# Kernel tuning notes

Measured on AMD Instinct MI355X. Metric: run time of the kernel, lower is better.

## Reference

```python
import jax, jax.numpy as jnp
import numpy as np

D_MODEL = 1024
N_LAYERS = 2
D_STATE = 64
D_CONV = 4
EXPAND = 2
D_INNER = EXPAND * D_MODEL            # 2048
HEADDIM = D_STATE                     # 64 (headdim=d_state per module code)
NHEADS = D_INNER // HEADDIM           # 32
CONV_DIM = D_INNER + 2 * D_STATE      # 2176 (ngroups=1)
D_IN_PROJ = 2 * D_INNER + 2 * D_STATE + NHEADS  # 4256
EPS = 1e-5


def setup_inputs() -> dict:
    key = jax.random.key(0)
    ks = jax.random.split(key, 8)
    B, L = 2, 4096
    return {
        "x": jax.random.normal(ks[0], (B, L, D_MODEL), jnp.float32),
        "ln_w": jnp.ones((N_LAYERS, D_MODEL), jnp.float32),
        "ln_b": jnp.zeros((N_LAYERS, D_MODEL), jnp.float32),
        "in_proj_w": jax.random.normal(ks[1], (N_LAYERS, D_IN_PROJ, D_MODEL), jnp.float32) * (D_MODEL ** -0.5),
        "conv_w": jax.random.normal(ks[2], (N_LAYERS, CONV_DIM, D_CONV), jnp.float32) * (D_CONV ** -0.5),
        "conv_b": jnp.zeros((N_LAYERS, CONV_DIM), jnp.float32),
        "dt_bias": jax.random.normal(ks[3], (N_LAYERS, NHEADS), jnp.float32) * 0.5,
        "A_log": jnp.log(jax.random.uniform(ks[4], (N_LAYERS, NHEADS), jnp.float32, 1.0, 16.0)),
        "D": jnp.ones((N_LAYERS, NHEADS), jnp.float32),
        "rms_w": jnp.ones((N_LAYERS, D_INNER), jnp.float32),
        "out_proj_w": jax.random.normal(ks[5], (N_LAYERS, D_MODEL, D_INNER), jnp.float32) * (D_INNER ** -0.5),
    }


def _layernorm(x, w, b):
    m = x.mean(-1, keepdims=True)
    v = ((x - m) ** 2).mean(-1, keepdims=True)
    return (x - m) * jax.lax.rsqrt(v + EPS) * w + b


def _mamba2(u, in_w, conv_w, conv_b, dt_bias, A_log, Dp, rms_w, out_w):
    b, l, _ = u.shape
    zxbcdt = u @ in_w.T                                   # (b,l,D_IN_PROJ)
    z, xBC, dt = jnp.split(zxbcdt, [D_INNER, D_INNER + CONV_DIM], axis=-1)
    dt = jax.nn.softplus(dt + dt_bias)                    # (b,l,H)
    # causal depthwise conv over sequence
    xBC = jnp.transpose(xBC, (0, 2, 1))                   # (b,C,l)
    xBC = jax.lax.conv_general_dilated(
        xBC, conv_w[:, None, :], (1,), [(D_CONV - 1, 0)],
        dimension_numbers=("NCH", "OIH", "NCH"), feature_group_count=CONV_DIM)
    xBC = jnp.transpose(xBC, (0, 2, 1)) + conv_b
    xBC = jax.nn.silu(xBC)
    xh, Bm, Cm = jnp.split(xBC, [D_INNER, D_INNER + D_STATE], axis=-1)
    xh = xh.reshape(b, l, NHEADS, HEADDIM)                # (b,l,H,P)
    A = -jnp.exp(A_log)                                   # (H,)
    dA = jnp.exp(dt * A)                                  # (b,l,H)

    def step(state, inputs):
        dA_t, dt_t, x_t, B_t, C_t = inputs                # (b,H),(b,H),(b,H,P),(b,N),(b,N)
        state = dA_t[:, :, None, None] * state + (dt_t[:, :, None] * x_t)[..., None] * B_t[:, None, None, :]
        y_t = jnp.einsum("bhpn,bn->bhp", state, C_t)
        return state, y_t

    xs = (jnp.moveaxis(dA, 1, 0), jnp.moveaxis(dt, 1, 0), jnp.moveaxis(xh, 1, 0),
          jnp.moveaxis(Bm, 1, 0), jnp.moveaxis(Cm, 1, 0))
    init = jnp.zeros((b, NHEADS, HEADDIM, D_STATE), u.dtype)
    _, ys = jax.lax.scan(step, init, xs)                  # ys: (l,b,H,P)
    y = jnp.moveaxis(ys, 0, 1) + Dp[None, None, :, None] * xh
    y = y.reshape(b, l, D_INNER)
    # gated RMSNorm (norm_before_gate=False): gate then rmsnorm
    y = y * jax.nn.silu(z)
    y = y * jax.lax.rsqrt(jnp.mean(y * y, -1, keepdims=True) + EPS) * rms_w
    return y @ out_w.T


def reference(x, ln_w, ln_b, in_proj_w, conv_w, conv_b, dt_bias, A_log, D, rms_w, out_proj_w):
    h = x
    for i in range(N_LAYERS):
        res = h
        h = _layernorm(h, ln_w[i], ln_b[i])
        h = _mamba2(h, in_proj_w[i], conv_w[i], conv_b[i], dt_bias[i], A_log[i], D[i], rms_w[i], out_proj_w[i])
        h = h + res
    return h
```

## Files before the change

kernel.cpp:

```cpp
#include <hip/hip_runtime.h>
#include <stdint.h>

#define D_MODEL   1024
#define D_STATE   64
#define D_INNER   2048
#define NHEADS    32
#define CONV_DIM  2176
#define D_IN_PROJ 4256
#define NPAD1     4352
#define LSEQ      4096
#define BL        8192
#define NCHUNK    32
#define TCH       128
#define EPS       1e-5f

typedef __attribute__((ext_vector_type(8))) _Float16 f16x8;
typedef __attribute__((ext_vector_type(4))) _Float16 f16x4;
typedef __attribute__((ext_vector_type(4))) float f32x4;

__device__ __forceinline__ void load_lds16(const void* g, void* l) {
  __builtin_amdgcn_global_load_lds((const __attribute__((address_space(1))) void*)g,
                                   (__attribute__((address_space(3))) void*)l, 16, 0, 0);
}

__global__ __launch_bounds__(256) void cvt_w1_kernel(const float* __restrict__ w,
                                                     _Float16* __restrict__ o) {
  size_t idx = (size_t)blockIdx.x * 256 + threadIdx.x;
  int k = idx & 1023;
  size_t nr = idx >> 10;
  int layer = (int)(nr / NPAD1);
  int n = (int)(nr % NPAD1);
  float v = (n < D_IN_PROJ) ? w[((size_t)layer * D_IN_PROJ + n) * 1024 + k] : 0.f;
  o[idx] = (_Float16)v;
}
__global__ __launch_bounds__(256) void cvt_w2_kernel(const float* __restrict__ w,
                                                     _Float16* __restrict__ o) {
  size_t idx = (size_t)blockIdx.x * 256 + threadIdx.x;
  o[idx] = (_Float16)w[idx];
}

__global__ __launch_bounds__(256) void ln_kernel(const float* __restrict__ x,
                                                 const float* __restrict__ w,
                                                 const float* __restrict__ b,
                                                 _Float16* __restrict__ o) {
  int row = blockIdx.x, tid = threadIdx.x;
  const float* xr = x + (size_t)row * D_MODEL;
  float4 v = *(const float4*)(xr + tid * 4);
  float s = v.x + v.y + v.z + v.w;
  float q = v.x * v.x + v.y * v.y + v.z * v.z + v.w * v.w;
  for (int off = 1; off < 64; off <<= 1) { s += __shfl_xor(s, off); q += __shfl_xor(q, off); }
  __shared__ float rs[4], rq[4];
  int wave = tid >> 6, lane = tid & 63;
  if (lane == 0) { rs[wave] = s; rq[wave] = q; }
  __syncthreads();
  s = rs[0] + rs[1] + rs[2] + rs[3];
  q = rq[0] + rq[1] + rq[2] + rq[3];
  float mean = s * (1.f / D_MODEL);
  float var = q * (1.f / D_MODEL) - mean * mean;
  float rstd = rsqrtf(var + EPS);
  int c = tid * 4;
  f16x4 ov;
  ov[0] = (_Float16)((v.x - mean) * rstd * w[c + 0] + b[c + 0]);
  ov[1] = (_Float16)((v.y - mean) * rstd * w[c + 1] + b[c + 1]);
  ov[2] = (_Float16)((v.z - mean) * rstd * w[c + 2] + b[c + 2]);
  ov[3] = (_Float16)((v.w - mean) * rstd * w[c + 3] + b[c + 3]);
  *(f16x4*)(o + (size_t)row * D_MODEL + c) = ov;
}

template <int MODE>
__global__ __launch_bounds__(512, 4) void gemm_f16_kernel(
    const _Float16* __restrict__ A, int lda,
    const _Float16* __restrict__ Bw, int K, int NBN, int NT,
    _Float16* __restrict__ Zb, _Float16* __restrict__ XPRE, float* __restrict__ AUX,
    float* __restrict__ Cf, const float* __restrict__ resid) {
  __shared__ _Float16 lA[3][256 * 32];
  __shared__ _Float16 lB[3][128 * 32];
  int tid = threadIdx.x;
  int wv = tid >> 6, lane = tid & 63;
  const int wm = (wv >> 1) * 64, wn = (wv & 1) * 64;
  const int fr = lane & 15;
  const int s4 = lane >> 4;
  int nwg = gridDim.x;
  int cpt = NT >> 3;
  int xcd = (int)blockIdx.x & 7;
  int step = nwg >> 3;

  for (int lt = (int)blockIdx.x >> 3; lt < cpt; lt += step) {
    int wg = xcd * cpt + lt;
    int band = wg / (4 * NBN), rem = wg % (4 * NBN);
    int bm = band * 4 + (rem & 3);
    int bn = rem >> 2;
    size_t aoff = (size_t)(bm * 256) * lda;
    size_t boff = (size_t)(bn * 128) * K;

    f32x4 acc[4][4];
    f32x4 zero = {0.f, 0.f, 0.f, 0.f};
#pragma unroll
    for (int i = 0; i < 4; ++i)
#pragma unroll
      for (int j = 0; j < 4; ++j) acc[i][j] = zero;

    auto stage = [&](int k0, int buf) {
#pragma unroll
      for (int c = 0; c < 2; ++c) {
        int row = (wv * 2 + c) * 16 + (lane >> 2);
        int col = k0 + (((lane & 3) ^ ((row >> 1) & 3)) << 3);
        load_lds16(A + aoff + (size_t)row * lda + col,
                   &lA[buf][(wv * 2 + c) * 512 + lane * 8]);
      }
      int rowb = wv * 16 + (lane >> 2);
      int colb = k0 + (((lane & 3) ^ ((rowb >> 1) & 3)) << 3);
      load_lds16(Bw + boff + (size_t)rowb * K + colb, &lB[buf][wv * 512 + lane * 8]);
    };

    int nk = K >> 5;
    stage(0, 0);
    stage(32, 1);
    int cur = 0;
    for (int kk = 0; kk < nk; ++kk) {
      if (kk + 2 < nk) {
        int sb = cur + 2; if (sb >= 3) sb -= 3;
        stage((kk + 2) << 5, sb);
        asm volatile("s_waitcnt vmcnt(6)" ::: "memory");
      } else if (kk + 1 < nk) {
        asm volatile("s_waitcnt vmcnt(3)" ::: "memory");
      } else {
        asm volatile("s_waitcnt vmcnt(0)" ::: "memory");
      }
      __builtin_amdgcn_s_barrier();
      __builtin_amdgcn_sched_barrier(0);
      f16x8 af[4], bf[4];
#pragma unroll
      for (int i = 0; i < 4; ++i) {
        int R = wm + i * 16 + fr;
        af[i] = *(const f16x8*)&lA[cur][R * 32 + ((s4 ^ ((R >> 1) & 3)) << 3)];
      }
#pragma unroll
      for (int j = 0; j < 4; ++j) {
        int R = wn + j * 16 + fr;
        bf[j] = *(const f16x8*)&lB[cur][R * 32 + ((s4 ^ ((R >> 1) & 3)) << 3)];
      }
#pragma unroll
      for (int i = 0; i < 4; ++i)
#pragma unroll
        for (int j = 0; j < 4; ++j)
          acc[i][j] = __builtin_amdgcn_mfma_f32_16x16x32_f16(af[i], bf[j], acc[i][j], 0, 0, 0);
      __builtin_amdgcn_sched_barrier(0);
      __builtin_amdgcn_s_barrier();
      cur = cur + 1; if (cur >= 3) cur = 0;
    }

    int r0 = (lane >> 4) * 4;
    int cc = lane & 15;
#pragma unroll
    for (int i = 0; i < 4; ++i) {
#pragma unroll
      for (int j = 0; j < 4; ++j) {
        int col = bn * 128 + wn + j * 16 + cc;
#pragma unroll
        for (int r = 0; r < 4; ++r) {
          size_t row = (size_t)(bm * 256 + wm + i * 16 + r0 + r);
          float v = acc[i][j][r];
          if constexpr (MODE == 0) {
            if (col < 2048)       Zb[row * 2048 + col] = (_Float16)v;
            else if (col < 4096)  XPRE[row * 2048 + (col - 2048)] = (_Float16)v;
            else if (col < 4256)  AUX[row * 160 + (col - 4096)] = v;
          } else {
            size_t idx = row * 1024 + col;
            Cf[idx] = v + resid[idx];
          }
        }
      }
    }
  }
}

__global__ __launch_bounds__(128) void dtlc_kernel(const float* __restrict__ aux,
                                                   const float* __restrict__ dtb,
                                                   const float* __restrict__ alog,
                                                   float* __restrict__ dtt,
                                                   float* __restrict__ lco) {
  int bid = blockIdx.x;
  int h = bid >> 6, b = (bid >> 5) & 1, ct = bid & 31;
  int tid = threadIdx.x, lane = tid & 63;
  int l = b * LSEQ + ct * TCH + tid;
  float A = -__expf(alog[h]);
  float v = aux[(size_t)l * 160 + 128 + h] + dtb[h];
  float sp = (v > 20.f) ? v : log1pf(expf(v));
  size_t base = (size_t)h * BL + b * LSEQ + ct * TCH;
  dtt[base + tid] = sp;
  float d = sp * A;
#pragma unroll
  for (int off = 1; off < 64; off <<= 1) {
    float o = __shfl_up(d, off);
    if (lane >= off) d += o;
  }
  __shared__ float tot;
  if (tid == 63) tot = d;
  __syncthreads();
  if (tid >= 64) d += tot;
  lco[base + tid] = d;
}

__global__ __launch_bounds__(256) void conv_kernel(const _Float16* __restrict__ xpre,
                                                   const float* __restrict__ aux,
                                                   const float* __restrict__ cw,
                                                   const float* __restrict__ cb,
                                                   _Float16* __restrict__ xt,
                                                   _Float16* __restrict__ cbh,
                                                   _Float16* __restrict__ bt) {
  int c = blockIdx.y * 256 + threadIdx.x;
  if (c >= CONV_DIM) return;
  int l0 = blockIdx.x * 16;
  float w0 = cw[c * 4 + 0], w1 = cw[c * 4 + 1], w2 = cw[c * 4 + 2], w3 = cw[c * 4 + 3];
  float bias = cb[c];
  bool isx = (c < 2048);
  auto ldx = [&](int l) -> float {
    return isx ? (float)xpre[(size_t)l * 2048 + c] : aux[(size_t)l * 160 + (c - 2048)];
  };
  float a0 = 0.f, a1 = 0.f, a2 = 0.f;
  if ((l0 & 4095) != 0) { a0 = ldx(l0 - 3); a1 = ldx(l0 - 2); a2 = ldx(l0 - 1); }
  _Float16 ob[16];
#pragma unroll
  for (int t = 0; t < 16; ++t) {
    int l = l0 + t;
    float a3 = ldx(l);
    float acc = bias + a0 * w0 + a1 * w1 + a2 * w2 + a3 * w3;
    acc = acc / (1.f + __expf(-acc));
    ob[t] = (_Float16)acc;
    if (!isx) cbh[(size_t)l * 128 + (c - 2048)] = ob[t];
    a0 = a1; a1 = a2; a2 = a3;
  }
  f16x8 v0, v1;
#pragma unroll
  for (int j = 0; j < 8; ++j) { v0[j] = ob[j]; v1[j] = ob[8 + j]; }
  if (isx) {
    *(f16x8*)&xt[(size_t)c * 8192 + l0] = v0;
    *(f16x8*)&xt[(size_t)c * 8192 + l0 + 8] = v1;
  } else if (c < 2112) {
    *(f16x8*)&bt[(size_t)(c - 2048) * 8192 + l0] = v0;
    *(f16x8*)&bt[(size_t)(c - 2048) * 8192 + l0 + 8] = v1;
  }
}

__global__ __launch_bounds__(256) void scan_state_kernel(
    const _Float16* __restrict__ xt, const _Float16* __restrict__ bt,
    const float* __restrict__ lc, const float* __restrict__ dtt,
    float* __restrict__ cs) {
  int bid = blockIdx.x;
  int chunk = bid & 31, h = (bid >> 5) & 31, b = bid >> 10;
  int tid = threadIdx.x;
  size_t gb = (size_t)b * LSEQ + chunk * TCH;
  size_t cdb = (size_t)h * BL + gb;
  __shared__ _Float16 xtl[64 * 128];
  __shared__ _Float16 btl[64 * 128];
  __shared__ float ldsW[128];
  if (tid < 128) ldsW[tid] = dtt[cdb + tid] * __expf(lc[cdb + 127] - lc[cdb + tid]);
  __syncthreads();
  int rr = tid >> 4, cl = tid & 15;
#pragma unroll
  for (int p = 0; p < 4; ++p) {
    int row = p * 16 + rr;
    f16x8 v = *(const f16x8*)&xt[(size_t)(h * 64 + row) * BL + gb + cl * 8];
    f16x8 bv = *(const f16x8*)&bt[(size_t)row * BL + gb + cl * 8];
    f16x8 sv;
#pragma unroll
    for (int j = 0; j < 8; ++j) sv[j] = (_Float16)((float)v[j] * ldsW[cl * 8 + j]);
    int byo = (row * 256 + cl * 16) ^ ((row & 7) << 4);
    *(f16x8*)((char*)xtl + byo) = sv;
    *(f16x8*)((char*)btl + byo) = bv;
  }
  __syncthreads();
  int wv = tid >> 6, lane = tid & 63;
  int fr = lane & 15, fk = (lane >> 4) * 8, r0 = (lane >> 4) * 4, cc = lane & 15;
  int swz = (fr & 7) << 4;
  f32x4 acc[4];
  f32x4 zero = {0.f, 0.f, 0.f, 0.f};
#pragma unroll
  for (int j = 0; j < 4; ++j) acc[j] = zero;
#pragma unroll
  for (int k0 = 0; k0 < 128; k0 += 32) {
    f16x8 af = *(const f16x8*)((char*)xtl + (((wv * 16 + fr) * 256 + (k0 + fk) * 2) ^ swz));
#pragma unroll
    for (int j = 0; j < 4; ++j) {
      f16x8 bf = *(const f16x8*)((char*)btl + (((j * 16 + fr) * 256 + (k0 + fk) * 2) ^ swz));
      acc[j] = __builtin_amdgcn_mfma_f32_16x16x32_f16(af, bf, acc[j], 0, 0, 0);
    }
  }
  size_t cbase = (((size_t)(b * 32 + h) * 32) + chunk) * 4096;
#pragma unroll
  for (int j = 0; j < 4; ++j)
#pragma unroll
    for (int r = 0; r < 4; ++r)
      cs[cbase + (wv * 16 + r0 + r) * 64 + j * 16 + cc] = acc[j][r];
}

__global__ __launch_bounds__(256) void scan_p2_kernel(float* __restrict__ cs,
                                                      const float* __restrict__ lc) {
  int bid = blockIdx.x;
  int b = bid >> 7, h = (bid >> 2) & 31, pq = bid & 3;
  int tid = threadIdx.x;
  size_t base = ((size_t)(b * 32 + h) * 32) * 4096 + (size_t)(pq * 256 + tid) * 4;
  const float* lcd = lc + (size_t)h * BL + b * LSEQ;
  float4 s = {0.f, 0.f, 0.f, 0.f};
  for (int c = 0; c < NCHUNK; ++c) {
    size_t idx = base + (size_t)c * 4096;
    float4 e = *(const float4*)&cs[idx];
    float P = __expf(lcd[c * TCH + TCH - 1]);
    *(float4*)&cs[idx] = s;
    s.x = e.x + P * s.x;
    s.y = e.y + P * s.y;
    s.z = e.z + P * s.z;
    s.w = e.w + P * s.w;
  }
}

__global__ __launch_bounds__(256) void scan_y_kernel(
    const _Float16* __restrict__ xt, const _Float16* __restrict__ cbh,
    const float* __restrict__ cs, const float* __restrict__ lc,
    const float* __restrict__ dtt, const float* __restrict__ Dv,
    _Float16* __restrict__ y) {
  int bid = blockIdx.x;
  int chunk = bid & 31, h = (bid >> 5) & 31, b = bid >> 10;
  int tid = threadIdx.x;
  size_t gb = (size_t)b * LSEQ + chunk * TCH;
  size_t cdb = (size_t)h * BL + gb;

  __shared__ _Float16 uCB[2 * 128 * 64];
  __shared__ _Float16 xtl[64 * 128];
  __shared__ _Float16 spl[64 * 64];
  __shared__ float ldsLc[128];
  __shared__ float ldsDt[128];
  _Float16* Cl = uCB;
  _Float16* Bl = uCB + 128 * 64;
  _Float16* Pl = uCB;

  int rr = tid >> 4, cl = tid & 15;
#pragma unroll
  for (int p = 0; p < 8; ++p) {
    int row = p * 16 + rr;
    f16x8 v = *(const f16x8*)&cbh[(gb + row) * 128 + cl * 8];
    int byo = (row * 128 + (cl & 7) * 16) ^ ((row & 7) << 4);
    if (cl < 8) *(f16x8*)((char*)Bl + byo) = v;
    else        *(f16x8*)((char*)Cl + byo) = v;
  }
  size_t cbase = (((size_t)(b * 32 + h) * 32) + chunk) * 4096;
#pragma unroll
  for (int p = 0; p < 4; ++p) {
    int row = p * 16 + rr;
    f16x8 v = *(const f16x8*)&xt[(size_t)(h * 64 + row) * BL + gb + cl * 8];
    int byo = (row * 256 + cl * 16) ^ ((row & 7) << 4);
    *(f16x8*)((char*)xtl + byo) = v;
    float4 sv = *(const float4*)&cs[cbase + row * 64 + cl * 4];
    f16x4 sh = {(_Float16)sv.x, (_Float16)sv.y, (_Float16)sv.z, (_Float16)sv.w};
    int byo2 = (row * 128 + cl * 8) ^ ((row & 7) << 4);
    *(f16x4*)((char*)spl + byo2) = sh;
  }
  if (tid < 128) { ldsLc[tid] = lc[cdb + tid]; ldsDt[tid] = dtt[cdb + tid]; }
  __syncthreads();

  int wv = tid >> 6, lane = tid & 63;
  int fr = lane & 15, fk = (lane >> 4) * 8, r0 = (lane >> 4) * 4, cc = lane & 15;
  int tb = wv * 32;
  int swz = (fr & 7) << 4;

  f32x4 accY[2][4];
  f32x4 accS[2][8];
  f32x4 zero = {0.f, 0.f, 0.f, 0.f};
#pragma unroll
  for (int i = 0; i < 2; ++i) {
#pragma unroll
    for (int j = 0; j < 4; ++j) accY[i][j] = zero;
#pragma unroll
    for (int j = 0; j < 8; ++j) accS[i][j] = zero;
  }

#pragma unroll
  for (int k0 = 0; k0 < 64; k0 += 32) {
    f16x8 ac[2];
#pragma unroll
    for (int i = 0; i < 2; ++i)
      ac[i] = *(const f16x8*)((char*)Cl + (((tb + i * 16 + fr) * 128 + (k0 + fk) * 2) ^ swz));
#pragma unroll
    for (int j = 0; j < 4; ++j) {
      f16x8 bs = *(const f16x8*)((char*)spl + (((j * 16 + fr) * 128 + (k0 + fk) * 2) ^ swz));
#pragma unroll
      for (int i = 0; i < 2; ++i)
        accY[i][j] = __builtin_amdgcn_mfma_f32_16x16x32_f16(ac[i], bs, accY[i][j], 0, 0, 0);
    }
#pragma unroll
    for (int j = 0; j < 8; ++j) {
      f16x8 bb = *(const f16x8*)((char*)Bl + (((j * 16 + fr) * 128 + (k0 + fk) * 2) ^ swz));
#pragma unroll
      for (int i = 0; i < 2; ++i)
        accS[i][j] = __builtin_amdgcn_mfma_f32_16x16x32_f16(ac[i], bb, accS[i][j], 0, 0, 0);
    }
  }

  float lct[2][4];
#pragma unroll
  for (int i = 0; i < 2; ++i)
#pragma unroll
    for (int r = 0; r < 4; ++r) lct[i][r] = ldsLc[tb + i * 16 + r0 + r];
#pragma unroll
  for (int i = 0; i < 2; ++i)
#pragma unroll
    for (int r = 0; r < 4; ++r) {
      float sc = __expf(lct[i][r]);
#pragma unroll
      for (int j = 0; j < 4; ++j) accY[i][j][r] *= sc;
    }

  __syncthreads();
  float Dh = Dv[h];
#pragma unroll
  for (int i = 0; i < 2; ++i)
#pragma unroll
    for (int jj = 0; jj < 8; ++jj) {
      int s = jj * 16 + cc;
      float lcs = ldsLc[s];
      float dts = ldsDt[s];
#pragma unroll
      for (int r = 0; r < 4; ++r) {
        int t = tb + i * 16 + r0 + r;
        float v = 0.f;
        if (s <= t) v = accS[i][jj][r] * __expf(lct[i][r] - lcs) * dts;
        if (s == t) v += Dh;
        int byo = (t * 256 + s * 2) ^ ((t & 7) << 4);
        *(_Float16*)((char*)Pl + byo) = (_Float16)v;
      }
    }
  __syncthreads();

#pragma unroll
  for (int k0 = 0; k0 < 128; k0 += 32) {
    f16x8 ap[2];
#pragma unroll
    for (int i = 0; i < 2; ++i)
      ap[i] = *(const f16x8*)((char*)Pl + (((tb + i * 16 + fr) * 256 + (k0 + fk) * 2) ^ swz));
#pragma unroll
    for (int j = 0; j < 4; ++j) {
      f16x8 bx = *(const f16x8*)((char*)xtl + (((j * 16 + fr) * 256 + (k0 + fk) * 2) ^ swz));
#pragma unroll
      for (int i = 0; i < 2; ++i)
        accY[i][j] = __builtin_amdgcn_mfma_f32_16x16x32_f16(ap[i], bx, accY[i][j], 0, 0, 0);
    }
  }

#pragma unroll
  for (int i = 0; i < 2; ++i)
#pragma unroll
    for (int j = 0; j < 4; ++j)
#pragma unroll
      for (int r = 0; r < 4; ++r) {
        int t = tb + i * 16 + r0 + r;
        y[(gb + t) * 2048 + h * 64 + j * 16 + cc] = (_Float16)accY[i][j][r];
      }
}

__global__ __launch_bounds__(256) void gate_rms_kernel(const _Float16* __restrict__ yf,
                                                       const _Float16* __restrict__ zb,
                                                       const float* __restrict__ rw,
                                                       _Float16* __restrict__ g) {
  int row = blockIdx.x, tid = threadIdx.x;
  int c0 = tid * 8;
  f16x8 yv = *(const f16x8*)(yf + (size_t)row * D_INNER + c0);
  f16x8 zv = *(const f16x8*)(zb + (size_t)row * D_INNER + c0);
  float gv[8];
  float q = 0.f;
#pragma unroll
  for (int u = 0; u < 8; ++u) {
    float yy = (float)yv[u];
    float zz = (float)zv[u];
    float t = yy * (zz / (1.f + __expf(-zz)));
    gv[u] = t;
    q += t * t;
  }
  for (int off = 1; off < 64; off <<= 1) q += __shfl_xor(q, off);
  __shared__ float rq[4];
  if ((tid & 63) == 0) rq[tid >> 6] = q;
  __syncthreads();
  q = rq[0] + rq[1] + rq[2] + rq[3];
  float scale = rsqrtf(q * (1.f / D_INNER) + EPS);
  float4 r0 = *(const float4*)&rw[c0];
  float4 r1 = *(const float4*)&rw[c0 + 4];
  f16x8 o;
  o[0] = (_Float16)(gv[0] * scale * r0.x);
  o[1] = (_Float16)(gv[1] * scale * r0.y);
  o[2] = (_Float16)(gv[2] * scale * r0.z);
  o[3] = (_Float16)(gv[3] * scale * r0.w);
  o[4] = (_Float16)(gv[4] * scale * r1.x);
  o[5] = (_Float16)(gv[5] * scale * r1.y);
  o[6] = (_Float16)(gv[6] * scale * r1.z);
  o[7] = (_Float16)(gv[7] * scale * r1.w);
  *(f16x8*)(g + (size_t)row * D_INNER + c0) = o;
}

extern "C" void kernel_launch(void* const* d_in, const int* in_sizes, int n_in,
                              void* d_out, int out_size, void* d_ws, size_t ws_size,
                              hipStream_t stream) {
  (void)in_sizes; (void)n_in; (void)out_size; (void)ws_size;
  const float* x     = (const float*)d_in[0];
  const float* ln_w  = (const float*)d_in[1];
  const float* ln_b  = (const float*)d_in[2];
  const float* w_in  = (const float*)d_in[3];
  const float* cw    = (const float*)d_in[4];
  const float* cb    = (const float*)d_in[5];
  const float* dtb   = (const float*)d_in[6];
  const float* alog  = (const float*)d_in[7];
  const float* dvec  = (const float*)d_in[8];
  const float* rmsw  = (const float*)d_in[9];
  const float* w_out = (const float*)d_in[10];
  float* out = (float*)d_out;

  char* ws = (char*)d_ws;
  size_t off = 0;
  auto alloc = [&](size_t bytes) -> char* {
    char* p = ws + off;
    off += (bytes + 255) & ~(size_t)255;
    return p;
  };
  _Float16* W1 = (_Float16*)alloc(2ull * 2 * NPAD1 * 1024);
  _Float16* W2 = (_Float16*)alloc(2ull * 2 * 1024 * 2048);
  char* REGION = alloc(4ull * BL * D_INNER);
  _Float16* LNf = (_Float16*)REGION;
  _Float16* Yf = (_Float16*)REGION;
  _Float16* Zb = (_Float16*)alloc(2ull * BL * D_INNER);
  _Float16* XPRE = (_Float16*)alloc(2ull * BL * D_INNER);
  _Float16* XT = (_Float16*)alloc(2ull * BL * D_INNER);
  float* AUX  = (float*)alloc(4ull * BL * 160);
  _Float16* CB16 = (_Float16*)alloc(2ull * BL * 128);
  float* DTt = (float*)alloc(4ull * NHEADS * BL);
  float* LC  = (float*)alloc(4ull * NHEADS * BL);
  _Float16* BT = (_Float16*)alloc(2ull * D_STATE * BL);
  float* CS = (float*)alloc(4ull * 2 * NHEADS * NCHUNK * 4096);

  cvt_w1_kernel<<<(2 * NPAD1 * 1024) / 256, 256, 0, stream>>>(w_in, W1);
  cvt_w2_kernel<<<(2 * 1024 * 2048) / 256, 256, 0, stream>>>(w_out, W2);

  for (int layer = 0; layer < 2; ++layer) {
    const float* hin = layer ? (const float*)out : x;
    size_t o1 = (size_t)layer * NPAD1 * 1024;
    size_t o2 = (size_t)layer * 1024 * 2048;
    ln_kernel<<<BL, 256, 0, stream>>>(hin, ln_w + layer * D_MODEL, ln_b + layer * D_MODEL, LNf);
    gemm_f16_kernel<0><<<512, 512, 0, stream>>>(
        LNf, 1024, W1 + o1, 1024, NPAD1 / 128, (8192 / 256) * (NPAD1 / 128),
        Zb, XPRE, AUX, nullptr, nullptr);
    dtlc_kernel<<<2048, 128, 0, stream>>>(AUX, dtb + layer * NHEADS,
                                          alog + layer * NHEADS, DTt, LC);
    conv_kernel<<<dim3(BL / 16, 9), 256, 0, stream>>>(XPRE, AUX, cw + layer * CONV_DIM * 4,
                                                      cb + layer * CONV_DIM, XT, CB16, BT);
    scan_state_kernel<<<2048, 256, 0, stream>>>(XT, BT, LC, DTt, CS);
    scan_p2_kernel<<<256, 256, 0, stream>>>(CS, LC);
    scan_y_kernel<<<2048, 256, 0, stream>>>(XT, CB16, CS, LC, DTt,
                                            dvec + layer * NHEADS, Yf);
    gate_rms_kernel<<<BL, 256, 0, stream>>>(Yf, Zb, rmsw + layer * D_INNER, Zb);
    gemm_f16_kernel<1><<<256, 512, 0, stream>>>(
        Zb, 2048, W2 + o2, 2048, 1024 / 128, (8192 / 256) * (1024 / 128),
        nullptr, nullptr, nullptr, out, hin);
  }
}
```

Measured before the change: 760.1 us.

## Use one tile per GEMM workgroup and LDS-transposed coalesced conv output

The GEMM kernels drop the persistent tile loop and launch one workgroup per output tile, with the XCD-aware tile mapping computed directly from blockIdx. This removes loop overhead and lets the hardware scheduler balance tiles across CUs. The conv kernel now handles 64 timesteps per thread and stages results in a padded LDS tile, then writes the transposed xt/bt outputs as coalesced 16-byte vectors instead of scattered per-channel strided stores. Each conv thread does more serial work, so there are fewer blocks and longer per-thread loops.

```diff
diff --git a/kernel.cpp b/kernel.cpp
--- a/kernel.cpp
+++ b/kernel.cpp
@@ -70,105 +70,101 @@
 template <int MODE>
 __global__ __launch_bounds__(512, 4) void gemm_f16_kernel(
     const _Float16* __restrict__ A, int lda,
-    const _Float16* __restrict__ Bw, int K, int NBN, int NT,
+    const _Float16* __restrict__ Bw, int K, int NBN,
     _Float16* __restrict__ Zb, _Float16* __restrict__ XPRE, float* __restrict__ AUX,
     float* __restrict__ Cf, const float* __restrict__ resid) {
   __shared__ _Float16 lA[3][256 * 32];
   __shared__ _Float16 lB[3][128 * 32];
   int tid = threadIdx.x;
   int wv = tid >> 6, lane = tid & 63;
+  int nwg = gridDim.x;
+  int cpx = nwg >> 3;
+  int wg = ((int)blockIdx.x & 7) * cpx + ((int)blockIdx.x >> 3);
+  int band = wg / (4 * NBN), rem = wg % (4 * NBN);
+  int bm = band * 4 + (rem & 3);
+  int bn = rem >> 2;
+
   const int wm = (wv >> 1) * 64, wn = (wv & 1) * 64;
   const int fr = lane & 15;
   const int s4 = lane >> 4;
-  int nwg = gridDim.x;
-  int cpt = NT >> 3;
-  int xcd = (int)blockIdx.x & 7;
-  int step = nwg >> 3;
-
-  for (int lt = (int)blockIdx.x >> 3; lt < cpt; lt += step) {
-    int wg = xcd * cpt + lt;
-    int band = wg / (4 * NBN), rem = wg % (4 * NBN);
-    int bm = band * 4 + (rem & 3);
-    int bn = rem >> 2;
-    size_t aoff = (size_t)(bm * 256) * lda;
-    size_t boff = (size_t)(bn * 128) * K;
-
-    f32x4 acc[4][4];
-    f32x4 zero = {0.f, 0.f, 0.f, 0.f};
+  size_t aoff = (size_t)(bm * 256) * lda;
+  size_t boff = (size_t)(bn * 128) * K;
+
+  f32x4 acc[4][4];
+  f32x4 zero = {0.f, 0.f, 0.f, 0.f};
+#pragma unroll
+  for (int i = 0; i < 4; ++i)
+#pragma unroll
+    for (int j = 0; j < 4; ++j) acc[i][j] = zero;
+
+  auto stage = [&](int k0, int buf) {
+#pragma unroll
+    for (int c = 0; c < 2; ++c) {
+      int row = (wv * 2 + c) * 16 + (lane >> 2);
+      int col = k0 + (((lane & 3) ^ ((row >> 1) & 3)) << 3);
+      load_lds16(A + aoff + (size_t)row * lda + col,
+                 &lA[buf][(wv * 2 + c) * 512 + lane * 8]);
+    }
+    int rowb = wv * 16 + (lane >> 2);
+    int colb = k0 + (((lane & 3) ^ ((rowb >> 1) & 3)) << 3);
+    load_lds16(Bw + boff + (size_t)rowb * K + colb, &lB[buf][wv * 512 + lane * 8]);
+  };
+
+  int nk = K >> 5;
+  stage(0, 0);
+  stage(32, 1);
+  int cur = 0;
+  for (int kk = 0; kk < nk; ++kk) {
+    if (kk + 2 < nk) {
+      int sb = cur + 2; if (sb >= 3) sb -= 3;
+      stage((kk + 2) << 5, sb);
+      asm volatile("s_waitcnt vmcnt(6)" ::: "memory");
+    } else if (kk + 1 < nk) {
+      asm volatile("s_waitcnt vmcnt(3)" ::: "memory");
+    } else {
+      asm volatile("s_waitcnt vmcnt(0)" ::: "memory");
+    }
+    __builtin_amdgcn_s_barrier();
+    __builtin_amdgcn_sched_barrier(0);
+    f16x8 af[4], bf[4];
+#pragma unroll
+    for (int i = 0; i < 4; ++i) {
+      int R = wm + i * 16 + fr;
+      af[i] = *(const f16x8*)&lA[cur][R * 32 + ((s4 ^ ((R >> 1) & 3)) << 3)];
+    }
+#pragma unroll
+    for (int j = 0; j < 4; ++j) {
+      int R = wn + j * 16 + fr;
+      bf[j] = *(const f16x8*)&lB[cur][R * 32 + ((s4 ^ ((R >> 1) & 3)) << 3)];
+    }
 #pragma unroll
     for (int i = 0; i < 4; ++i)
 #pragma unroll
-      for (int j = 0; j < 4; ++j) acc[i][j] = zero;
-
-    auto stage = [&](int k0, int buf) {
-#pragma unroll
-      for (int c = 0; c < 2; ++c) {
-        int row = (wv * 2 + c) * 16 + (lane >> 2);
-        int col = k0 + (((lane & 3) ^ ((row >> 1) & 3)) << 3);
-        load_lds16(A + aoff + (size_t)row * lda + col,
-                   &lA[buf][(wv * 2 + c) * 512 + lane * 8]);
-      }
-      int rowb = wv * 16 + (lane >> 2);
-      int colb = k0 + (((lane & 3) ^ ((rowb >> 1) & 3)) << 3);
-      load_lds16(Bw + boff + (size_t)rowb * K + colb, &lB[buf][wv * 512 + lane * 8]);
-    };
-
-    int nk = K >> 5;
-    stage(0, 0);
-    stage(32, 1);
-    int cur = 0;
-    for (int kk = 0; kk < nk; ++kk) {
-      if (kk + 2 < nk) {
-        int sb = cur + 2; if (sb >= 3) sb -= 3;
-        stage((kk + 2) << 5, sb);
-        asm volatile("s_waitcnt vmcnt(6)" ::: "memory");
-      } else if (kk + 1 < nk) {
-        asm volatile("s_waitcnt vmcnt(3)" ::: "memory");
-      } else {
-        asm volatile("s_waitcnt vmcnt(0)" ::: "memory");
-      }
-      __builtin_amdgcn_s_barrier();
-      __builtin_amdgcn_sched_barrier(0);
-      f16x8 af[4], bf[4];
-#pragma unroll
-      for (int i = 0; i < 4; ++i) {
-        int R = wm + i * 16 + fr;
-        af[i] = *(const f16x8*)&lA[cur][R * 32 + ((s4 ^ ((R >> 1) & 3)) << 3)];
-      }
-#pragma unroll
-      for (int j = 0; j < 4; ++j) {
-        int R = wn + j * 16 + fr;
-        bf[j] = *(const f16x8*)&lB[cur][R * 32 + ((s4 ^ ((R >> 1) & 3)) << 3)];
-      }
-#pragma unroll
-      for (int i = 0; i < 4; ++i)
-#pragma unroll
-        for (int j = 0; j < 4; ++j)
-          acc[i][j] = __builtin_amdgcn_mfma_f32_16x16x32_f16(af[i], bf[j], acc[i][j], 0, 0, 0);
-      __builtin_amdgcn_sched_barrier(0);
-      __builtin_amdgcn_s_barrier();
-      cur = cur + 1; if (cur >= 3) cur = 0;
-    }
-
-    int r0 = (lane >> 4) * 4;
-    int cc = lane & 15;
-#pragma unroll
-    for (int i = 0; i < 4; ++i) {
-#pragma unroll
-      for (int j = 0; j < 4; ++j) {
-        int col = bn * 128 + wn + j * 16 + cc;
-#pragma unroll
-        for (int r = 0; r < 4; ++r) {
-          size_t row = (size_t)(bm * 256 + wm + i * 16 + r0 + r);
-          float v = acc[i][j][r];
-          if constexpr (MODE == 0) {
-            if (col < 2048)       Zb[row * 2048 + col] = (_Float16)v;
-            else if (col < 4096)  XPRE[row * 2048 + (col - 2048)] = (_Float16)v;
-            else if (col < 4256)  AUX[row * 160 + (col - 4096)] = v;
-          } else {
-            size_t idx = row * 1024 + col;
-            Cf[idx] = v + resid[idx];
-          }
+      for (int j = 0; j < 4; ++j)
+        acc[i][j] = __builtin_amdgcn_mfma_f32_16x16x32_f16(af[i], bf[j], acc[i][j], 0, 0, 0);
+    __builtin_amdgcn_sched_barrier(0);
+    __builtin_amdgcn_s_barrier();
+    cur = cur + 1; if (cur >= 3) cur = 0;
+  }
+
+  int r0 = (lane >> 4) * 4;
+  int cc = lane & 15;
+#pragma unroll
+  for (int i = 0; i < 4; ++i) {
+#pragma unroll
+    for (int j = 0; j < 4; ++j) {
+      int col = bn * 128 + wn + j * 16 + cc;
+#pragma unroll
+      for (int r = 0; r < 4; ++r) {
+        size_t row = (size_t)(bm * 256 + wm + i * 16 + r0 + r);
+        float v = acc[i][j][r];
+        if constexpr (MODE == 0) {
+          if (col < 2048)       Zb[row * 2048 + col] = (_Float16)v;
+          else if (col < 4096)  XPRE[row * 2048 + (col - 2048)] = (_Float16)v;
+          else if (col < 4256)  AUX[row * 160 + (col - 4096)] = v;
+        } else {
+          size_t idx = row * 1024 + col;
+          Cf[idx] = v + resid[idx];
         }
       }
     }
@@ -209,37 +205,54 @@
                                                    _Float16* __restrict__ xt,
                                                    _Float16* __restrict__ cbh,
                                                    _Float16* __restrict__ bt) {
-  int c = blockIdx.y * 256 + threadIdx.x;
-  if (c >= CONV_DIM) return;
-  int l0 = blockIdx.x * 16;
-  float w0 = cw[c * 4 + 0], w1 = cw[c * 4 + 1], w2 = cw[c * 4 + 2], w3 = cw[c * 4 + 3];
-  float bias = cb[c];
+  __shared__ _Float16 T[256 * 70];
+  int tid = threadIdx.x;
+  int c = blockIdx.y * 256 + tid;
+  bool active = (c < CONV_DIM);
+  int l0 = blockIdx.x * 64;
+  float w0 = 0.f, w1 = 0.f, w2 = 0.f, w3 = 0.f, bias = 0.f;
   bool isx = (c < 2048);
+  if (active) {
+    w0 = cw[c * 4 + 0]; w1 = cw[c * 4 + 1]; w2 = cw[c * 4 + 2]; w3 = cw[c * 4 + 3];
+    bias = cb[c];
+  }
   auto ldx = [&](int l) -> float {
     return isx ? (float)xpre[(size_t)l * 2048 + c] : aux[(size_t)l * 160 + (c - 2048)];
   };
   float a0 = 0.f, a1 = 0.f, a2 = 0.f;
-  if ((l0 & 4095) != 0) { a0 = ldx(l0 - 3); a1 = ldx(l0 - 2); a2 = ldx(l0 - 1); }
-  _Float16 ob[16];
-#pragma unroll
-  for (int t = 0; t < 16; ++t) {
-    int l = l0 + t;
-    float a3 = ldx(l);
-    float acc = bias + a0 * w0 + a1 * w1 + a2 * w2 + a3 * w3;
-    acc = acc / (1.f + __expf(-acc));
-    ob[t] = (_Float16)acc;
-    if (!isx) cbh[(size_t)l * 128 + (c - 2048)] = ob[t];
-    a0 = a1; a1 = a2; a2 = a3;
-  }
-  f16x8 v0, v1;
-#pragma unroll
-  for (int j = 0; j < 8; ++j) { v0[j] = ob[j]; v1[j] = ob[8 + j]; }
-  if (isx) {
-    *(f16x8*)&xt[(size_t)c * 8192 + l0] = v0;
-    *(f16x8*)&xt[(size_t)c * 8192 + l0 + 8] = v1;
-  } else if (c < 2112) {
-    *(f16x8*)&bt[(size_t)(c - 2048) * 8192 + l0] = v0;
-    *(f16x8*)&bt[(size_t)(c - 2048) * 8192 + l0 + 8] = v1;
+  if (active && (l0 & 4095) != 0) { a0 = ldx(l0 - 3); a1 = ldx(l0 - 2); a2 = ldx(l0 - 1); }
+  for (int t = 0; t < 64; ++t) {
+    if (active) {
+      int l = l0 + t;
+      float a3 = ldx(l);
+      float acc = bias + a0 * w0 + a1 * w1 + a2 * w2 + a3 * w3;
+      acc = acc / (1.f + __expf(-acc));
+      T[tid * 70 + t] = (_Float16)acc;
+      if (!isx) cbh[(size_t)l * 128 + (c - 2048)] = (_Float16)acc;
+      a0 = a1; a1 = a2; a2 = a3;
+    }
+  }
+  __syncthreads();
+  int u = tid >> 3, lg = tid & 7;
+  if (blockIdx.y < 8) {
+#pragma unroll
+    for (int p = 0; p < 8; ++p) {
+      int cl2 = p * 32 + u;
+      int cg = blockIdx.y * 256 + cl2;
+      f16x8 v;
+#pragma unroll
+      for (int j = 0; j < 8; ++j) v[j] = T[cl2 * 70 + lg * 8 + j];
+      *(f16x8*)&xt[(size_t)cg * 8192 + l0 + lg * 8] = v;
+    }
+  } else {
+#pragma unroll
+    for (int p = 0; p < 2; ++p) {
+      int cl2 = p * 32 + u;
+      f16x8 v;
+#pragma unroll
+      for (int j = 0; j < 8; ++j) v[j] = T[cl2 * 70 + lg * 8 + j];
+      *(f16x8*)&bt[(size_t)cl2 * 8192 + l0 + lg * 8] = v;
+    }
   }
 }
 
@@ -543,20 +556,18 @@
     size_t o1 = (size_t)layer * NPAD1 * 1024;
     size_t o2 = (size_t)layer * 1024 * 2048;
     ln_kernel<<<BL, 256, 0, stream>>>(hin, ln_w + layer * D_MODEL, ln_b + layer * D_MODEL, LNf);
-    gemm_f16_kernel<0><<<512, 512, 0, stream>>>(
-        LNf, 1024, W1 + o1, 1024, NPAD1 / 128, (8192 / 256) * (NPAD1 / 128),
-        Zb, XPRE, AUX, nullptr, nullptr);
+    gemm_f16_kernel<0><<<dim3((8192 / 256) * (NPAD1 / 128)), 512, 0, stream>>>(
+        LNf, 1024, W1 + o1, 1024, NPAD1 / 128, Zb, XPRE, AUX, nullptr, nullptr);
     dtlc_kernel<<<2048, 128, 0, stream>>>(AUX, dtb + layer * NHEADS,
                                           alog + layer * NHEADS, DTt, LC);
-    conv_kernel<<<dim3(BL / 16, 9), 256, 0, stream>>>(XPRE, AUX, cw + layer * CONV_DIM * 4,
+    conv_kernel<<<dim3(BL / 64, 9), 256, 0, stream>>>(XPRE, AUX, cw + layer * CONV_DIM * 4,
                                                       cb + layer * CONV_DIM, XT, CB16, BT);
     scan_state_kernel<<<2048, 256, 0, stream>>>(XT, BT, LC, DTt, CS);
     scan_p2_kernel<<<256, 256, 0, stream>>>(CS, LC);
     scan_y_kernel<<<2048, 256, 0, stream>>>(XT, CB16, CS, LC, DTt,
                                             dvec + layer * NHEADS, Yf);
     gate_rms_kernel<<<BL, 256, 0, stream>>>(Yf, Zb, rmsw + layer * D_INNER, Zb);
-    gemm_f16_kernel<1><<<256, 512, 0, stream>>>(
-        Zb, 2048, W2 + o2, 2048, 1024 / 128, (8192 / 256) * (1024 / 128),
-        nullptr, nullptr, nullptr, out, hin);
-  }
-}
+    gemm_f16_kernel<1><<<dim3((8192 / 256) * (1024 / 128)), 512, 0, stream>>>(
+        Zb, 2048, W2 + o2, 2048, 1024 / 128, nullptr, nullptr, nullptr, out, hin);
+  }
+}
```

Result: no change. 770.4 us, median of 2 (+1.4%).
